# Performance work log

Measured on AMD Instinct MI355X. Metric: run time of the kernel, lower is better.

The kernel has to match this reference:

```python
import jax, jax.numpy as jnp
import numpy as np

RES = 128  # hparams.data_res


def _grid_points(res):
    x_ = np.linspace(-15, 15, res)
    X, Y = np.meshgrid(x_, x_)
    return jnp.asarray(np.stack((X.flatten(), Y.flatten())).T, dtype=jnp.float32)  # [P=res^2, 2]


def setup_inputs() -> dict:
    key = jax.random.key(0)
    k1, k2 = jax.random.split(key)
    BS, T = 16, 64
    mu = jax.random.normal(k1, (BS, T, 2), dtype=jnp.float32) * 3.0
    # SPD covariance per (BS, T): A @ A^T + 0.5 I
    A = jax.random.normal(k2, (BS, T, 2, 2), dtype=jnp.float32)
    covar = jnp.einsum('btij,btkj->btik', A, A) + 0.5 * jnp.eye(2, dtype=jnp.float32)
    return {"mu": mu, "covar": covar}


def reference(mu, covar):
    # mu: [BS, T, 2], covar: [BS, T, 2, 2]
    BS, T, _ = mu.shape
    points = _grid_points(RES)  # [P, 2]
    # Closed-form 2x2 Gaussian log-prob (what MultivariateNormal computes via Cholesky)
    a = covar[..., 0, 0]
    b = covar[..., 0, 1]
    c = covar[..., 1, 0]
    d = covar[..., 1, 1]
    det = a * d - b * c  # [BS, T]
    diff = points[:, None, None, :] - mu[None]  # [P, BS, T, 2]
    dx = diff[..., 0]
    dy = diff[..., 1]
    # quadratic form (p-mu)^T Sigma^{-1} (p-mu) with Sigma^{-1} = [[d,-b],[-c,a]]/det
    q = (d * dx * dx - (b + c) * dx * dy + a * dy * dy) / det  # [P, BS, T]
    log_two_pi = jnp.log(jnp.asarray(2.0 * np.pi, dtype=mu.dtype))
    logp = -log_two_pi - 0.5 * jnp.log(det) - 0.5 * q  # [P, BS, T]
    probs = jnp.exp(logp)
    # permute(1,2,0).reshape(BS, T, 1, RES, RES)
    probs = jnp.transpose(probs, (1, 2, 0)).reshape(BS, T, 1, RES, RES)
    flat = probs.reshape(BS, T, -1)
    mn = flat.min(axis=-1)[..., None, None, None]
    mx = flat.max(axis=-1)[..., None, None, None]
    return (probs - mn) / (mx - mn)
```

## Files before the change

kernel.cpp:

```cpp
#include <hip/hip_runtime.h>

#define RES 128
#define NPT (RES * RES)

__global__ __launch_bounds__(256) void AnalyticalDecoder_85581518340204_kernel(
    const float* __restrict__ mu,
    const float* __restrict__ covar,
    float* __restrict__ out)
{
    const int bt  = blockIdx.x;
    const int tid = threadIdx.x;

    const float mux = mu[bt * 2 + 0];
    const float muy = mu[bt * 2 + 1];
    const float a = covar[bt * 4 + 0];
    const float b = covar[bt * 4 + 1];
    const float c = covar[bt * 4 + 2];
    const float d = covar[bt * 4 + 3];
    const float det     = a * d - b * c;
    const float inv_det = 1.0f / det;

    const float step = 30.0f / 127.0f;

    const int j0 = (tid & 31) * 4;
    float A0[4], A1[4];
    const float A2 = a * inv_det;
    #pragma unroll
    for (int e = 0; e < 4; ++e) {
        const float px = -15.0f + (float)(j0 + e) * step;
        const float dx = px - mux;
        A0[e] = d * dx * dx * inv_det;
        A1[e] = -(b + c) * dx * inv_det;
    }

    const int i0 = tid >> 5;
    float p[16][4];
    float mn = 3.4e38f, mx = -3.4e38f;
    #pragma unroll
    for (int it = 0; it < 16; ++it) {
        const int   i  = it * 8 + i0;
        const float py = -15.0f + (float)i * step;
        const float dy = py - muy;
        const float t1 = A2 * dy;
        #pragma unroll
        for (int e = 0; e < 4; ++e) {
            const float q = A0[e] + dy * (A1[e] + t1);
            const float v = __expf(-0.5f * q);
            p[it][e] = v;
            mn = fminf(mn, v);
            mx = fmaxf(mx, v);
        }
    }

    #pragma unroll
    for (int off = 32; off > 0; off >>= 1) {
        mn = fminf(mn, __shfl_xor(mn, off));
        mx = fmaxf(mx, __shfl_xor(mx, off));
    }
    __shared__ float smn[4], smx[4];
    const int wave = tid >> 6;
    if ((tid & 63) == 0) { smn[wave] = mn; smx[wave] = mx; }
    __syncthreads();
    mn = fminf(fminf(smn[0], smn[1]), fminf(smn[2], smn[3]));
    mx = fmaxf(fmaxf(smx[0], smx[1]), fmaxf(smx[2], smx[3]));

    const float inv = 1.0f / (mx - mn);

    float4* out4 = (float4*)(out + (size_t)bt * NPT);
    #pragma unroll
    for (int it = 0; it < 16; ++it) {
        float4 v;
        v.x = (p[it][0] - mn) * inv;
        v.y = (p[it][1] - mn) * inv;
        v.z = (p[it][2] - mn) * inv;
        v.w = (p[it][3] - mn) * inv;
        out4[it * 256 + tid] = v;
    }
}

extern "C" void kernel_launch(void* const* d_in, const int* in_sizes, int n_in,
                              void* d_out, int out_size, void* d_ws, size_t ws_size,
                              hipStream_t stream) {
    const float* mu    = (const float*)d_in[0];
    const float* covar = (const float*)d_in[1];
    float* out = (float*)d_out;
    const int n_bt = in_sizes[0] / 2;
    AnalyticalDecoder_85581518340204_kernel<<<n_bt, 256, 0, stream>>>(mu, covar, out);
}
```

Before: 17.38 us.

## Compute min/max analytically and split each Gaussian map across two blocks

Instead of evaluating the whole 128x128 grid and reducing it to find min and max, the kernel now finds them in closed form. The minimum comes from the four grid corners, where the convex quadratic form is largest. The maximum comes from the two grid columns nearest each row's analytic optimum, reduced across 128 rows. This removes the 64-value register buffer and lets each (batch,time) map be split across two blocks, doubling the grid to improve occupancy and parallelism. The exp is folded into exp2 with log2e prescaled constants. The analytic extrema depend on the grid sampling matching the reference exactly, and any rounding differences could slightly change the normalisation.

```diff
diff --git a/kernel.cpp b/kernel.cpp
--- a/kernel.cpp
+++ b/kernel.cpp
@@ -8,8 +8,10 @@
     const float* __restrict__ covar,
     float* __restrict__ out)
 {
-    const int bt  = blockIdx.x;
-    const int tid = threadIdx.x;
+    const int bid  = blockIdx.x;
+    const int bt   = bid >> 1;
+    const int half = bid & 1;
+    const int tid  = threadIdx.x;
 
     const float mux = mu[bt * 2 + 0];
     const float muy = mu[bt * 2 + 1];
@@ -17,63 +19,74 @@
     const float b = covar[bt * 4 + 1];
     const float c = covar[bt * 4 + 2];
     const float d = covar[bt * 4 + 3];
-    const float det     = a * d - b * c;
-    const float inv_det = 1.0f / det;
+    const float det = a * d - b * c;
 
-    const float step = 30.0f / 127.0f;
+    const float LOG2E = 1.4426950408889634f;
+    const float ninv2 = -0.5f * LOG2E / det;
+    const float Kd  = ninv2 * d;
+    const float Kbc = -ninv2 * (b + c);
+    const float Ka  = ninv2 * a;
 
-    const int j0 = (tid & 31) * 4;
-    float A0[4], A1[4];
-    const float A2 = a * inv_det;
+    const float step    = 30.0f / 127.0f;
+    const float invstep = 127.0f / 30.0f;
+
+    const int   r   = tid & 127;
+    const float dyr = (-15.0f + (float)r * step) - muy;
+    const float dxs = (b + c) * dyr / (2.0f * d);
+    const float jc  = (mux + dxs + 15.0f) * invstep;
+    int k0 = (int)floorf(jc);
+    k0 = max(0, min(126, k0));
+    const float dx0 = (-15.0f + (float)k0 * step) - mux;
+    const float dx1 = dx0 + step;
+    const float dyr2 = Ka * dyr * dyr;
+    const float s0 = Kd * dx0 * dx0 + Kbc * dx0 * dyr + dyr2;
+    const float s1 = Kd * dx1 * dx1 + Kbc * dx1 * dyr + dyr2;
+    float smax = fmaxf(s0, s1);
+
+    float smin = 3.4e38f;
     #pragma unroll
-    for (int e = 0; e < 4; ++e) {
-        const float px = -15.0f + (float)(j0 + e) * step;
-        const float dx = px - mux;
-        A0[e] = d * dx * dx * inv_det;
-        A1[e] = -(b + c) * dx * inv_det;
-    }
-
-    const int i0 = tid >> 5;
-    float p[16][4];
-    float mn = 3.4e38f, mx = -3.4e38f;
-    #pragma unroll
-    for (int it = 0; it < 16; ++it) {
-        const int   i  = it * 8 + i0;
-        const float py = -15.0f + (float)i * step;
-        const float dy = py - muy;
-        const float t1 = A2 * dy;
+    for (int ci = 0; ci < 2; ++ci) {
+        const float dyc = (ci ? 15.0f : -15.0f) - muy;
         #pragma unroll
-        for (int e = 0; e < 4; ++e) {
-            const float q = A0[e] + dy * (A1[e] + t1);
-            const float v = __expf(-0.5f * q);
-            p[it][e] = v;
-            mn = fminf(mn, v);
-            mx = fmaxf(mx, v);
+        for (int cj = 0; cj < 2; ++cj) {
+            const float dxc = (cj ? 15.0f : -15.0f) - mux;
+            smin = fminf(smin, Kd * dxc * dxc + Kbc * dxc * dyc + Ka * dyc * dyc);
         }
     }
 
     #pragma unroll
-    for (int off = 32; off > 0; off >>= 1) {
-        mn = fminf(mn, __shfl_xor(mn, off));
-        mx = fmaxf(mx, __shfl_xor(mx, off));
+    for (int off = 32; off > 0; off >>= 1)
+        smax = fmaxf(smax, __shfl_xor(smax, off));
+    __shared__ float sm[4];
+    const int wave = tid >> 6;
+    if ((tid & 63) == 0) sm[wave] = smax;
+    __syncthreads();
+    smax = fmaxf(fmaxf(sm[0], sm[1]), fmaxf(sm[2], sm[3]));
+
+    const float mxp = exp2f(smax);
+    const float mnp = exp2f(smin);
+    const float inv = 1.0f / (mxp - mnp);
+
+    const int j0 = (tid & 31) * 4;
+    float C0[4], C1[4];
+    #pragma unroll
+    for (int e = 0; e < 4; ++e) {
+        const float dx = (-15.0f + (float)(j0 + e) * step) - mux;
+        C0[e] = Kd * dx * dx;
+        C1[e] = Kbc * dx;
     }
-    __shared__ float smn[4], smx[4];
-    const int wave = tid >> 6;
-    if ((tid & 63) == 0) { smn[wave] = mn; smx[wave] = mx; }
-    __syncthreads();
-    mn = fminf(fminf(smn[0], smn[1]), fminf(smn[2], smn[3]));
-    mx = fmaxf(fmaxf(smx[0], smx[1]), fmaxf(smx[2], smx[3]));
-
-    const float inv = 1.0f / (mx - mn);
-
-    float4* out4 = (float4*)(out + (size_t)bt * NPT);
+    const int i0 = tid >> 5;
+    float4* out4 = (float4*)(out + (size_t)bt * NPT + half * (NPT / 2));
     #pragma unroll
-    for (int it = 0; it < 16; ++it) {
+    for (int it = 0; it < 8; ++it) {
+        const int   i  = half * 64 + it * 8 + i0;
+        const float dy = (-15.0f + (float)i * step) - muy;
+        const float t1 = Ka * dy;
         float4 v;
-        v.x = (p[it][0] - mn) * inv;
-        v.y = (p[it][1] - mn) * inv;
-        v.z = (p[it][2] - mn) * inv;
-        v.w = (p[it][3] - mn) * inv;
+        v.x = (exp2f(C0[0] + dy * (C1[0] + t1)) - mnp) * inv;
+        v.y = (exp2f(C0[1] + dy * (C1[1] + t1)) - mnp) * inv;
+        v.z = (exp2f(C0[2] + dy * (C1[2] + t1)) - mnp) * inv;
+        v.w = (exp2f(C0[3] + dy * (C1[3] + t1)) - mnp) * inv;
         out4[it * 256 + tid] = v;
     }
 }
@@ -85,5 +98,5 @@
     const float* covar = (const float*)d_in[1];
     float* out = (float*)d_out;
     const int n_bt = in_sizes[0] / 2;
-    AnalyticalDecoder_85581518340204_kernel<<<n_bt, 256, 0, stream>>>(mu, covar, out);
+    AnalyticalDecoder_85581518340204_kernel<<<n_bt * 2, 256, 0, stream>>>(mu, covar, out);
 }
```

After: 17.48 us. About the same (+0.5%).
